# Optimization experiments

Hardware: AMD Instinct MI355X
Metric: run time of the kernel (lower is better)

The kernel has to match this reference:

```python
import jax, jax.numpy as jnp
import numpy as np

N = 50000       # nodes
DEG = 16        # fixed degree -> consistent CSR
E = N * DEG     # 800000 edges
IN_FEATS = 256
HEADS = 4
OUT_FEATS = 64
NEG_SLOPE = 0.2


def setup_inputs() -> dict:
    key = jax.random.key(0)
    kx, kc, kw, ki, kj = jax.random.split(key, 5)
    x = jax.random.normal(kx, (N, IN_FEATS), dtype=jnp.float32)
    # consistent CSR: every row has DEG neighbors
    row_id = jnp.repeat(jnp.arange(N, dtype=jnp.int64), DEG)          # [E] dst per edge
    row_ptr = jnp.arange(N + 1, dtype=jnp.int64) * DEG                # [N+1]
    col_id = jax.random.randint(kc, (E,), 0, N, dtype=jnp.int64)      # [E] src per edge
    # glorot-uniform parameters
    def glorot(k, shape, fan_in, fan_out):
        s = float(np.sqrt(6.0 / (fan_in + fan_out)))
        return jax.random.uniform(k, shape, jnp.float32, -s, s)
    W = glorot(kw, (HEADS * OUT_FEATS, IN_FEATS), IN_FEATS, HEADS * OUT_FEATS)  # nn.Linear weight
    att_i = glorot(ki, (1, HEADS, OUT_FEATS), HEADS, OUT_FEATS)
    att_j = glorot(kj, (1, HEADS, OUT_FEATS), HEADS, OUT_FEATS)
    return {"x": x, "row_id": row_id, "row_ptr": row_ptr, "col_id": col_id,
            "W": W, "att_i": att_i, "att_j": att_j}


def reference(x, row_id, row_ptr, col_id, W, att_i, att_j):
    n = x.shape[0]
    H, F = att_i.shape[1], att_i.shape[2]
    # node projection: [N, H, F]
    h = (x @ W.T).reshape(n, H, F)
    # per-node attention halves: [N, H]
    a_i = jnp.sum(h * att_i, axis=-1)   # destination term
    a_j = jnp.sum(h * att_j, axis=-1)   # source term
    # per-edge logits with leaky relu: [E, H]
    e = jax.nn.leaky_relu(a_i[row_id] + a_j[col_id], NEG_SLOPE)
    # segment-wise (per destination row) stable softmax
    m = jax.ops.segment_max(e, row_id, num_segments=n)
    m = jnp.where(jnp.isfinite(m), m, 0.0)
    p = jnp.exp(e - m[row_id])
    s = jax.ops.segment_sum(p, row_id, num_segments=n)
    alpha = p / (s[row_id] + 1e-16)                       # [E, H]
    # weighted scatter-sum of source features: [N, H, F]
    msg = h[col_id] * alpha[:, :, None]
    out = jax.ops.segment_sum(msg, row_id, num_segments=n)
    # concat heads
    return out.reshape(n, H * F)
```

## Files before the change

### kernel.cpp

```cpp
#include <hip/hip_runtime.h>
#include <hip/hip_bf16.h>
#include <stdint.h>

#define N_NODES 50000
#define DEG 16
#define IN_F 256
#define HEADS 4
#define OUT_F 64
#define HF 256
#define NEG_SLOPE 0.2f

typedef short bf16x8 __attribute__((ext_vector_type(8)));
typedef float f32x4 __attribute__((ext_vector_type(4)));

__device__ __forceinline__ unsigned short f2b(float f) {
    __hip_bfloat16 b = __float2bfloat16(f);
    return *(unsigned short*)&b;
}
__device__ __forceinline__ float b2f(unsigned short u) {
    union { uint32_t i; float f; } v; v.i = ((uint32_t)u) << 16;
    return v.f;
}

__global__ __launch_bounds__(256) void wprep(
    const float* __restrict__ W, unsigned short* __restrict__ Wbp)
{
    const int G = blockIdx.x * 256 + threadIdx.x;
    const int cb   = G >> 9;
    const int rem  = G & 511;
    const int kc8  = rem >> 6;
    const int lane = rem & 63;
    const int kg   = lane >> 4;
    const int ar   = lane & 15;
    const float* src = W + (size_t)(cb * 16 + ar) * IN_F + kc8 * 32 + kg * 8;
    float4 f0 = ((const float4*)src)[0];
    float4 f1 = ((const float4*)src)[1];
    bf16x8 v;
    v[0] = (short)f2b(f0.x); v[1] = (short)f2b(f0.y);
    v[2] = (short)f2b(f0.z); v[3] = (short)f2b(f0.w);
    v[4] = (short)f2b(f1.x); v[5] = (short)f2b(f1.y);
    v[6] = (short)f2b(f1.z); v[7] = (short)f2b(f1.w);
    *(bf16x8*)(Wbp + (size_t)G * 8) = v;
}

__global__ __launch_bounds__(256) void proj_fused(
    const float* __restrict__ x, const unsigned short* __restrict__ Wbp,
    const float* __restrict__ atti, const float* __restrict__ attj,
    unsigned short* __restrict__ h,
    float* __restrict__ a_i, float* __restrict__ a_j)
{
    __shared__ unsigned short As[32 * 256];

    const int tid  = threadIdx.x;
    const int lane = tid & 63;
    const int wave = tid >> 6;
    const int m0   = blockIdx.x * 32;

    #pragma unroll
    for (int p = 0; p < 4; p++) {
        const int C   = p * 256 + tid;
        const int row = C >> 5;
        const int c   = C & 31;
        int grow = m0 + row;
        if (grow >= N_NODES) grow = N_NODES - 1;
        const float* src = x + (size_t)grow * IN_F + c * 8;
        float4 f0 = ((const float4*)src)[0];
        float4 f1 = ((const float4*)src)[1];
        bf16x8 v;
        v[0] = (short)f2b(f0.x); v[1] = (short)f2b(f0.y);
        v[2] = (short)f2b(f0.z); v[3] = (short)f2b(f0.w);
        v[4] = (short)f2b(f1.x); v[5] = (short)f2b(f1.y);
        v[6] = (short)f2b(f1.z); v[7] = (short)f2b(f1.w);
        const int sc = c ^ (row & 7);
        *(bf16x8*)(As + row * 256 + sc * 8) = v;
    }
    __syncthreads();

    const int ar = lane & 15;
    const int kg = lane >> 4;
    const int ncol0 = wave * 64;

    f32x4 acc[2][4];
    #pragma unroll
    for (int i = 0; i < 2; i++)
        #pragma unroll
        for (int j = 0; j < 4; j++)
            #pragma unroll
            for (int k = 0; k < 4; k++) acc[i][j][k] = 0.0f;

    #pragma unroll
    for (int kc8 = 0; kc8 < 8; kc8++) {
        bf16x8 afrag[2], bfrag[4];
        #pragma unroll
        for (int mi = 0; mi < 2; mi++) {
            const int row = mi * 16 + ar;
            const int sc  = (kc8 * 4 + kg) ^ (row & 7);
            afrag[mi] = *(const bf16x8*)(As + row * 256 + sc * 8);
        }
        #pragma unroll
        for (int ni = 0; ni < 4; ni++) {
            const int cb = wave * 4 + ni;
            bfrag[ni] = *(const bf16x8*)(Wbp + ((size_t)(cb * 8 + kc8) * 64 + lane) * 8);
        }
        #pragma unroll
        for (int mi = 0; mi < 2; mi++)
            #pragma unroll
            for (int ni = 0; ni < 4; ni++)
                acc[mi][ni] = __builtin_amdgcn_mfma_f32_16x16x32_bf16(
                    afrag[mi], bfrag[ni], acc[mi][ni], 0, 0, 0);
    }

    float ai_l[4], aj_l[4];
    #pragma unroll
    for (int ni = 0; ni < 4; ni++) {
        ai_l[ni] = atti[ncol0 + ni * 16 + ar];
        aj_l[ni] = attj[ncol0 + ni * 16 + ar];
    }
    #pragma unroll
    for (int mi = 0; mi < 2; mi++) {
        #pragma unroll
        for (int reg = 0; reg < 4; reg++) {
            const int row = m0 + mi * 16 + kg * 4 + reg;
            float pi = 0.f, pj = 0.f;
            #pragma unroll
            for (int ni = 0; ni < 4; ni++) {
                const float v = acc[mi][ni][reg];
                pi += v * ai_l[ni];
                pj += v * aj_l[ni];
            }
            #pragma unroll
            for (int off = 1; off < 16; off <<= 1) {
                pi += __shfl_xor(pi, off);
                pj += __shfl_xor(pj, off);
            }
            if (row < N_NODES) {
                #pragma unroll
                for (int ni = 0; ni < 4; ni++)
                    h[(size_t)row * HF + ncol0 + ni * 16 + ar] = f2b(acc[mi][ni][reg]);
                if (ar == 0) {
                    a_i[row * HEADS + wave] = pi;
                    a_j[row * HEADS + wave] = pj;
                }
            }
        }
    }
}

__global__ __launch_bounds__(256, 8) void gat_agg3(
    const unsigned short* __restrict__ h,
    const float* __restrict__ a_i, const float* __restrict__ a_j,
    const int* __restrict__ col, float* __restrict__ out)
{
    const int bid  = blockIdx.x;
    const int head = (bid >> 1) & 3;
    const int idx  = ((bid >> 3) << 1) | (bid & 1);
    const int node = idx * 4 + (threadIdx.x >> 6);
    const int lane = threadIdx.x & 63;
    const int g    = lane >> 4;
    const int f    = lane & 15;

    const int src = col[node * DEG + f];
    float e = a_i[node * HEADS + head] + a_j[src * HEADS + head];
    e = (e > 0.0f) ? e : NEG_SLOPE * e;
    float p = __expf(e);
    float s = p;
    #pragma unroll
    for (int off = 1; off < 16; off <<= 1) s += __shfl_xor(s, off);
    const float alpha = p / (s + 1e-16f);

    int   sj[4];
    float al[4];
    #pragma unroll
    for (int i = 0; i < 4; i++) {
        sj[i] = __shfl(src,   4 * i + g);
        al[i] = __shfl(alpha, 4 * i + g);
    }
    ushort4 hv[4];
    #pragma unroll
    for (int i = 0; i < 4; i++)
        hv[i] = *(const ushort4*)(h + (size_t)sj[i] * HF + head * OUT_F + f * 4);

    float a0 = 0.f, a1 = 0.f, a2 = 0.f, a3 = 0.f;
    #pragma unroll
    for (int i = 0; i < 4; i++) {
        a0 += al[i] * b2f(hv[i].x);
        a1 += al[i] * b2f(hv[i].y);
        a2 += al[i] * b2f(hv[i].z);
        a3 += al[i] * b2f(hv[i].w);
    }
    #pragma unroll
    for (int off = 16; off < 64; off <<= 1) {
        a0 += __shfl_xor(a0, off);
        a1 += __shfl_xor(a1, off);
        a2 += __shfl_xor(a2, off);
        a3 += __shfl_xor(a3, off);
    }
    if (g == 0) {
        f32x4 o;
        o[0] = a0; o[1] = a1; o[2] = a2; o[3] = a3;
        __builtin_nontemporal_store(o,
            (f32x4*)(out + (size_t)node * HF + head * OUT_F + f * 4));
    }
}

extern "C" void kernel_launch(void* const* d_in, const int* in_sizes, int n_in,
                              void* d_out, int out_size, void* d_ws, size_t ws_size,
                              hipStream_t stream) {
    const float* x      = (const float*)d_in[0];
    const int*   col_id = (const int*)d_in[3];
    const float* W      = (const float*)d_in[4];
    const float* atti   = (const float*)d_in[5];
    const float* attj   = (const float*)d_in[6];
    float* out = (float*)d_out;

    unsigned short* h = (unsigned short*)d_ws;
    float* a_i = (float*)((char*)d_ws + (size_t)N_NODES * HF * 2);
    float* a_j = a_i + (size_t)N_NODES * HEADS;
    unsigned short* Wbp = (unsigned short*)(a_j + (size_t)N_NODES * HEADS);

    wprep<<<32, 256, 0, stream>>>(W, Wbp);
    proj_fused<<<(N_NODES + 31) / 32, 256, 0, stream>>>(x, Wbp, atti, attj, h, a_i, a_j);
    gat_agg3<<<N_NODES, 256, 0, stream>>>(h, a_i, a_j, col_id, out);
}
```

Before: 173.6 us.

## Assign one node per 16-lane group in aggregation, removing cross-group reduction

The aggregation kernel now has each 16-lane group own a whole destination node and loop over all 16 neighbors serially, instead of splitting neighbors across four lane groups and reducing with shuffles. Each wave therefore handles four nodes, and the grid shrinks from one block per node to about a quarter as many, with an early exit for padding blocks. This drops the cross-group shuffle reduction and the idle lanes at store time, and puts more independent gathers in flight per thread. The cost is higher register pressure from holding 16 gathered vectors, which could lower occupancy under the 8-block launch bound.

New measurement: 167.0 us. 1.04x faster.

```diff
diff --git a/kernel.cpp b/kernel.cpp
--- a/kernel.cpp
+++ b/kernel.cpp
@@ -146,7 +146,7 @@
     }
 }
 
-__global__ __launch_bounds__(256, 8) void gat_agg3(
+__global__ __launch_bounds__(256, 8) void gat_agg4(
     const unsigned short* __restrict__ h,
     const float* __restrict__ a_i, const float* __restrict__ a_j,
     const int* __restrict__ col, float* __restrict__ out)
@@ -154,10 +154,12 @@
     const int bid  = blockIdx.x;
     const int head = (bid >> 1) & 3;
     const int idx  = ((bid >> 3) << 1) | (bid & 1);
-    const int node = idx * 4 + (threadIdx.x >> 6);
+    if (idx >= 3125) return;
     const int lane = threadIdx.x & 63;
-    const int g    = lane >> 4;
+    const int wave = threadIdx.x >> 6;
+    const int n4   = lane >> 4;
     const int f    = lane & 15;
+    const int node = idx * 16 + wave * 4 + n4;
 
     const int src = col[node * DEG + f];
     float e = a_i[node * HEADS + head] + a_j[src * HEADS + head];
@@ -168,39 +170,33 @@
     for (int off = 1; off < 16; off <<= 1) s += __shfl_xor(s, off);
     const float alpha = p / (s + 1e-16f);
 
-    int   sj[4];
-    float al[4];
-    #pragma unroll
-    for (int i = 0; i < 4; i++) {
-        sj[i] = __shfl(src,   4 * i + g);
-        al[i] = __shfl(alpha, 4 * i + g);
-    }
-    ushort4 hv[4];
-    #pragma unroll
-    for (int i = 0; i < 4; i++)
-        hv[i] = *(const ushort4*)(h + (size_t)sj[i] * HF + head * OUT_F + f * 4);
+    const int b16 = n4 * 16;
+    int   sj[DEG];
+    float al[DEG];
+    #pragma unroll
+    for (int t = 0; t < DEG; t++) {
+        sj[t] = __shfl(src,   b16 + t);
+        al[t] = __shfl(alpha, b16 + t);
+    }
+
+    const unsigned short* hbase = h + head * OUT_F + f * 4;
+    ushort4 hv[DEG];
+    #pragma unroll
+    for (int t = 0; t < DEG; t++)
+        hv[t] = *(const ushort4*)(hbase + (size_t)sj[t] * HF);
 
     float a0 = 0.f, a1 = 0.f, a2 = 0.f, a3 = 0.f;
     #pragma unroll
-    for (int i = 0; i < 4; i++) {
-        a0 += al[i] * b2f(hv[i].x);
-        a1 += al[i] * b2f(hv[i].y);
-        a2 += al[i] * b2f(hv[i].z);
-        a3 += al[i] * b2f(hv[i].w);
-    }
-    #pragma unroll
-    for (int off = 16; off < 64; off <<= 1) {
-        a0 += __shfl_xor(a0, off);
-        a1 += __shfl_xor(a1, off);
-        a2 += __shfl_xor(a2, off);
-        a3 += __shfl_xor(a3, off);
-    }
-    if (g == 0) {
-        f32x4 o;
-        o[0] = a0; o[1] = a1; o[2] = a2; o[3] = a3;
-        __builtin_nontemporal_store(o,
-            (f32x4*)(out + (size_t)node * HF + head * OUT_F + f * 4));
-    }
+    for (int t = 0; t < DEG; t++) {
+        a0 += al[t] * b2f(hv[t].x);
+        a1 += al[t] * b2f(hv[t].y);
+        a2 += al[t] * b2f(hv[t].z);
+        a3 += al[t] * b2f(hv[t].w);
+    }
+    f32x4 o;
+    o[0] = a0; o[1] = a1; o[2] = a2; o[3] = a3;
+    __builtin_nontemporal_store(o,
+        (f32x4*)(out + (size_t)node * HF + head * OUT_F + f * 4));
 }
 
 extern "C" void kernel_launch(void* const* d_in, const int* in_sizes, int n_in,
@@ -220,5 +216,5 @@
 
     wprep<<<32, 256, 0, stream>>>(W, Wbp);
     proj_fused<<<(N_NODES + 31) / 32, 256, 0, stream>>>(x, Wbp, atti, attj, h, a_i, a_j);
-    gat_agg3<<<N_NODES, 256, 0, stream>>>(h, a_i, a_j, col_id, out);
-}
+    gat_agg4<<<12512, 256, 0, stream>>>(h, a_i, a_j, col_id, out);
+}
```
